# Performance work log

Measured on AMD Instinct MI355X. Metric: run time of the kernel, lower is better.

The kernel has to match this reference:

```python
import jax, jax.numpy as jnp
import numpy as np

K_NEIGHBOURS = 16
ITERATIONS = 3
NUM_CLASSES = 20
N_POINTS = 20000


def setup_inputs() -> dict:
    key = jax.random.key(0)
    k1, k2 = jax.random.split(key)
    logits = jax.random.normal(k1, (N_POINTS, NUM_CLASSES), dtype=jnp.float32)
    coords = jax.random.uniform(k2, (N_POINTS, 3), dtype=jnp.float32)
    # nn.init.eye_ then *= -0.1
    compat_w = (-0.1 * jnp.eye(NUM_CLASSES, dtype=jnp.float32))
    return {"logits": logits, "coords": coords, "compat_w": compat_w}


def _knn_graph(coords, k):
    # torch.cdist (p=2): euclidean distances, (N, N)
    sq = jnp.sum(coords * coords, axis=-1)
    d2 = sq[:, None] + sq[None, :] - 2.0 * (coords @ coords.T)
    dists = jnp.sqrt(jnp.clip(d2, 0.0))
    # smallest-k -> top_k of negated distances
    _, idx = jax.lax.top_k(-dists, k)  # (N, k)
    return idx


def reference(logits, coords, compat_w):
    knn_idx = _knn_graph(coords, K_NEIGHBOURS)
    q = jax.nn.softmax(logits, axis=-1)
    for _ in range(ITERATIONS):
        neighbour_q = q[knn_idx]            # (N, k, K) gather
        msg = jnp.mean(neighbour_q, axis=1)  # (N, K)
        refined = logits + msg @ compat_w.T  # nn.Linear: x @ W^T
        q = jax.nn.softmax(refined, axis=-1)
    return (refined, q)
```

## Files before the change

kernel.cpp:

```cpp
#include <hip/hip_runtime.h>

#define N_PTS 20000
#define NCLS 20
#define KNN 16
#define GRID 12
#define NCELLS (GRID * GRID * GRID)
#define HCELL (1.0f / (float)GRID)
#define CAND_CAP 512
#define KEY_CAP 128
#define R_TARGET 0.0680f

__device__ __forceinline__ int cell1d(float v) {
    int c = (int)(v * (float)GRID);
    return min(max(c, 0), GRID - 1);
}

__global__ __launch_bounds__(256) void count_scan_kernel(const float* __restrict__ coords,
                                                         int* __restrict__ cellCount,
                                                         int* __restrict__ doneCtr,
                                                         int* __restrict__ cellStart,
                                                         int* __restrict__ cellCursor) {
    const int p = blockIdx.x * blockDim.x + threadIdx.x;
    if (p < N_PTS) {
        const int cx = cell1d(coords[3 * p + 0]);
        const int cy = cell1d(coords[3 * p + 1]);
        const int cz = cell1d(coords[3 * p + 2]);
        atomicAdd(&cellCount[(cz * GRID + cy) * GRID + cx], 1);
    }
    __threadfence();
    __syncthreads();
    __shared__ bool isLast;
    if (threadIdx.x == 0)
        isLast = (atomicAdd(doneCtr, 1) == (int)gridDim.x - 1);
    __syncthreads();
    if (!isLast) return;

    __shared__ int part[256];
    const int t = threadIdx.x;
    const int base = t * 7;
    int local[7];
    int s = 0;
#pragma unroll
    for (int i = 0; i < 7; ++i) {
        const int c = base + i;
        const int v = (c < NCELLS)
            ? __hip_atomic_load(&cellCount[c], __ATOMIC_RELAXED, __HIP_MEMORY_SCOPE_AGENT)
            : 0;
        local[i] = s;
        s += v;
    }
    part[t] = s;
    __syncthreads();
    for (int off = 1; off < 256; off <<= 1) {
        const int v = part[t] + ((t >= off) ? part[t - off] : 0);
        __syncthreads();
        part[t] = v;
        __syncthreads();
    }
    const int excl = (t > 0) ? part[t - 1] : 0;
#pragma unroll
    for (int i = 0; i < 7; ++i) {
        const int c = base + i;
        if (c < NCELLS) {
            cellStart[c] = excl + local[i];
            cellCursor[c] = excl + local[i];
        }
    }
    if (t == 255) cellStart[NCELLS] = part[255];
}

__global__ __launch_bounds__(256) void scatter_kernel(const float* __restrict__ coords,
                                                      const float* __restrict__ logits,
                                                      int* __restrict__ cellCursor,
                                                      float4* __restrict__ sortedPts,
                                                      int* __restrict__ orig,
                                                      float* __restrict__ ls,
                                                      float* __restrict__ q0s) {
    const int p = blockIdx.x * blockDim.x + threadIdx.x;
    if (p >= N_PTS) return;
    const float x = coords[3 * p + 0];
    const float y = coords[3 * p + 1];
    const float z = coords[3 * p + 2];
    const int c = (cell1d(z) * GRID + cell1d(y)) * GRID + cell1d(x);
    const int pos = atomicAdd(&cellCursor[c], 1);
    sortedPts[pos] = make_float4(x, y, z, __uint_as_float((unsigned)p));
    orig[pos] = p;
    const float4* l4 = (const float4*)(logits + p * NCLS);
    float v[NCLS];
#pragma unroll
    for (int u = 0; u < 5; ++u) {
        const float4 a = l4[u];
        v[4 * u + 0] = a.x; v[4 * u + 1] = a.y;
        v[4 * u + 2] = a.z; v[4 * u + 3] = a.w;
    }
    float4* d4 = (float4*)(ls + pos * NCLS);
#pragma unroll
    for (int u = 0; u < 5; ++u)
        d4[u] = make_float4(v[4 * u], v[4 * u + 1], v[4 * u + 2], v[4 * u + 3]);
    float mx = v[0];
#pragma unroll
    for (int cc = 1; cc < NCLS; ++cc) mx = fmaxf(mx, v[cc]);
    float sum = 0.f;
#pragma unroll
    for (int cc = 0; cc < NCLS; ++cc) { v[cc] = __expf(v[cc] - mx); sum += v[cc]; }
    const float inv = 1.f / sum;
    float4* q4 = (float4*)(q0s + pos * NCLS);
#pragma unroll
    for (int u = 0; u < 5; ++u)
        q4[u] = make_float4(v[4 * u] * inv, v[4 * u + 1] * inv,
                            v[4 * u + 2] * inv, v[4 * u + 3] * inv);
}

__device__ void knn_ladder(const float4* __restrict__ sortedPts,
                           const int* __restrict__ cellStart,
                           const float4 qp, const int s, int hw,
                           unsigned long long* keys, const int lane,
                           int* __restrict__ knn_out) {
    const unsigned long long laneLt = (1ull << lane) - 1ull;
    const int cx = cell1d(qp.x), cy = cell1d(qp.y), cz = cell1d(qp.z);
    float g = 0.9995f * (float)hw * HCELL;
    float tau = g * g;
    int cnt = 0;
    for (int att = 0; att < 16; ++att) {
        cnt = 0;
        const int xlo = max(cx - hw, 0), xhi = min(cx + hw, GRID - 1);
        const int ylo = max(cy - hw, 0), yhi = min(cy + hw, GRID - 1);
        const int zlo = max(cz - hw, 0), zhi = min(cz + hw, GRID - 1);
        for (int zz = zlo; zz <= zhi; ++zz) {
            for (int yy = ylo; yy <= yhi; ++yy) {
                const int rowc = (zz * GRID + yy) * GRID;
                const int beg = cellStart[rowc + xlo];
                const int end = cellStart[rowc + xhi + 1];
                for (int j0 = beg; j0 < end; j0 += 64) {
                    const int j = j0 + lane;
                    const bool jv = j < end;
                    const float4 pt = sortedPts[jv ? j : beg];
                    const float dx = pt.x - qp.x, dy = pt.y - qp.y, dz = pt.z - qp.z;
                    const float d2 = dx * dx + dy * dy + dz * dz;
                    const bool take = jv && (d2 < tau);
                    const unsigned long long mm = __ballot(take);
                    if (take) {
                        const int pos = cnt + (int)__popcll(mm & laneLt);
                        if (pos < KEY_CAP)
                            keys[pos] = (((unsigned long long)__float_as_uint(d2)) << 32) |
                                        (unsigned long long)(unsigned)j;
                    }
                    cnt += (int)__popcll(mm);
                }
            }
        }
        if (cnt >= KNN && cnt <= KEY_CAP) break;
        if (cnt < KNN) {
            if (hw < GRID - 1) { ++hw; g = 0.9995f * (float)hw * HCELL; tau = g * g; }
            else tau *= 2.5f;
        } else {
            tau *= 0.6f;
        }
    }
    const int m = min(cnt, KEY_CAP);
    const unsigned long long k0 = (lane < m) ? keys[lane] : ~0ull;
    const unsigned long long k1 = (lane + 64 < m) ? keys[lane + 64] : ~0ull;
    int r0 = 0, r1 = 0;
    for (int j = 0; j < m; ++j) {
        const unsigned long long kj = keys[j];
        r0 += (kj < k0); r1 += (kj < k1);
    }
    if (lane < m && r0 < KNN)      knn_out[s * KNN + r0] = (int)(unsigned)(k0 & 0xffffffffull);
    if (lane + 64 < m && r1 < KNN) knn_out[s * KNN + r1] = (int)(unsigned)(k1 & 0xffffffffull);
}

__global__ __launch_bounds__(256) void knn_kernel(const float4* __restrict__ sortedPts,
                                                  const int* __restrict__ cellStart,
                                                  int* __restrict__ knn_out) {
    __shared__ float4 cand[CAND_CAP];
    __shared__ unsigned long long keys[4][KEY_CAP];
    const int lane = threadIdx.x & 63;
    const int wave = threadIdx.x >> 6;
    const int c = blockIdx.x >> 1;
    const int half = blockIdx.x & 1;
    const int cz = c / (GRID * GRID);
    const int cy = (c / GRID) % GRID;
    const int cx = c % GRID;
    const int pbeg = cellStart[c];
    const int pend = cellStart[c + 1];
    const int npts = pend - pbeg;
    if (npts <= 0) return;
    const unsigned long long laneLt = (1ull << lane) - 1ull;

    const int xlo = max(cx - 1, 0), xhi = min(cx + 1, GRID - 1);
    const int ylo = max(cy - 1, 0), yhi = min(cy + 1, GRID - 1);
    const int zlo = max(cz - 1, 0), zhi = min(cz + 1, GRID - 1);
    const int ny = yhi - ylo + 1;
    const int nruns = (zhi - zlo + 1) * ny;

    int beg = 0, len = 0;
    if (lane < nruns) {
        const int zz = zlo + lane / ny;
        const int yy = ylo + lane % ny;
        const int rowc = (zz * GRID + yy) * GRID;
        beg = cellStart[rowc + xlo];
        len = cellStart[rowc + xhi + 1] - beg;
    }
    int off = len;
#pragma unroll
    for (int sh = 1; sh < 16; sh <<= 1) {
        const int o = __shfl_up(off, sh, 64);
        if (lane >= sh) off += o;
    }
    const int nc = __shfl(off, nruns - 1);
    off -= len;
    const int ownRun = (cz - zlo) * ny + (cy - ylo);
    const int ownOff = __shfl(off, ownRun) + (pbeg - __shfl(beg, ownRun));

    if (nc <= CAND_CAP) {
        for (int r = wave; r < nruns; r += 4) {
            const int rb = __shfl(beg, r);
            const int rl = __shfl(len, r);
            const int ro = __shfl(off, r);
            for (int i = lane; i < rl; i += 64) {
                float4 pt = sortedPts[rb + i];
                pt.w = __uint_as_float((unsigned)(rb + i));
                cand[ro + i] = pt;
            }
        }
    }
    __syncthreads();

    if (nc > CAND_CAP) {
        for (int idx = 2 * wave + half; idx < npts; idx += 8)
            knn_ladder(sortedPts, cellStart, sortedPts[pbeg + idx], pbeg + idx,
                       2, keys[wave], lane, knn_out);
        return;
    }

    const float taumaxr = 0.9995f * HCELL;
    const float taumax = taumaxr * taumaxr;

    for (int idx = 2 * wave + half; idx < npts; idx += 8) {
        const int s = pbeg + idx;
        const float4 qp = cand[ownOff + idx];
        float r = R_TARGET;
        const float inv2r = 0.5f / r;
        const float fx = (fminf(qp.x + r, 1.f) - fmaxf(qp.x - r, 0.f)) * inv2r;
        const float fy = (fminf(qp.y + r, 1.f) - fmaxf(qp.y - r, 0.f)) * inv2r;
        const float fz = (fminf(qp.z + r, 1.f) - fmaxf(qp.z - r, 0.f)) * inv2r;
        const float f = fmaxf(fx * fy * fz, 0.05f);
        r = R_TARGET * __powf(f, -0.33333334f);
        float tau = fminf(r * r, taumax);
        bool triedMax = (tau >= taumax * 0.999f);

        int cnt = 0;
        bool ok = false;
        for (int att = 0; att < 5 && !ok; ++att) {
            cnt = 0;
            for (int j0 = 0; j0 < nc; j0 += 64) {
                const int j = j0 + lane;
                float d2 = 1e30f;
                unsigned pw = 0;
                if (j < nc) {
                    const float4 pt = cand[j];
                    const float dx = pt.x - qp.x, dy = pt.y - qp.y, dz = pt.z - qp.z;
                    d2 = dx * dx + dy * dy + dz * dz;
                    pw = __float_as_uint(pt.w);
                }
                const bool take = d2 < tau;
                const unsigned long long mm = __ballot(take);
                if (take) {
                    const int pos = cnt + (int)__popcll(mm & laneLt);
                    if (pos < KEY_CAP)
                        keys[wave][pos] =
                            (((unsigned long long)__float_as_uint(d2)) << 32) |
                            (unsigned long long)pw;
                }
                cnt += (int)__popcll(mm);
            }
            if (cnt >= KNN && cnt <= KEY_CAP) ok = true;
            else if (cnt < KNN) {
                if (triedMax) break;
                tau = taumax; triedMax = true;
            } else tau *= 0.6f;
        }
        if (!ok) {
            knn_ladder(sortedPts, cellStart, qp, s, 2, keys[wave], lane, knn_out);
            continue;
        }
        const int m = cnt;
        const unsigned long long k0 = (lane < m) ? keys[wave][lane] : ~0ull;
        const unsigned long long k1 = (lane + 64 < m) ? keys[wave][lane + 64] : ~0ull;
        int r0 = 0, r1 = 0;
        for (int j = 0; j < m; ++j) {
            const unsigned long long kj = keys[wave][j];
            r0 += (kj < k0); r1 += (kj < k1);
        }
        if (lane < m && r0 < KNN)      knn_out[s * KNN + r0] = (int)(unsigned)(k0 & 0xffffffffull);
        if (lane + 64 < m && r1 < KNN) knn_out[s * KNN + r1] = (int)(unsigned)(k1 & 0xffffffffull);
    }
}

__global__ __launch_bounds__(256) void crf_iter_kernel(const float* __restrict__ ls,
                                                       const float* __restrict__ W,
                                                       const int* __restrict__ knn,
                                                       const float* __restrict__ qin,
                                                       float* __restrict__ qout,
                                                       const int* __restrict__ orig,
                                                       float* __restrict__ outRef,
                                                       float* __restrict__ outQ) {
    __shared__ float Ws[NCLS * NCLS];
    for (int i = threadIdx.x; i < NCLS * NCLS; i += blockDim.x) Ws[i] = W[i];
    __syncthreads();
    const int t = blockIdx.x * blockDim.x + threadIdx.x;
    const int p = t >> 2;
    const int qtr = t & 3;
    if (p >= N_PTS) return;

    float acc[NCLS];
#pragma unroll
    for (int c = 0; c < NCLS; ++c) acc[c] = 0.f;

    const int4 k4 = ((const int4*)(knn + p * KNN))[qtr];
    const int ids[4] = {k4.x, k4.y, k4.z, k4.w};
#pragma unroll
    for (int u = 0; u < 4; ++u) {
        unsigned id = (unsigned)ids[u];
        if (id >= N_PTS) id = 0;
        const float4* r4 = (const float4*)(qin + id * NCLS);
#pragma unroll
        for (int v = 0; v < 5; ++v) {
            const float4 a = r4[v];
            acc[4 * v + 0] += a.x; acc[4 * v + 1] += a.y;
            acc[4 * v + 2] += a.z; acc[4 * v + 3] += a.w;
        }
    }
#pragma unroll
    for (int c = 0; c < NCLS; ++c) {
        acc[c] += __shfl_xor(acc[c], 1, 64);
        acc[c] += __shfl_xor(acc[c], 2, 64);
        acc[c] *= (1.f / 16.f);
    }

    const int c0 = qtr * 5;
    float ref[5];
#pragma unroll
    for (int i = 0; i < 5; ++i) {
        float s = ls[p * NCLS + c0 + i];
#pragma unroll
        for (int k = 0; k < NCLS; ++k) s += acc[k] * Ws[(c0 + i) * NCLS + k];
        ref[i] = s;
    }

    float mx = ref[0];
#pragma unroll
    for (int i = 1; i < 5; ++i) mx = fmaxf(mx, ref[i]);
    mx = fmaxf(mx, __shfl_xor(mx, 1, 64));
    mx = fmaxf(mx, __shfl_xor(mx, 2, 64));
    float ex[5];
    float ps = 0.f;
#pragma unroll
    for (int i = 0; i < 5; ++i) { ex[i] = __expf(ref[i] - mx); ps += ex[i]; }
    ps += __shfl_xor(ps, 1, 64);
    ps += __shfl_xor(ps, 2, 64);
    const float inv = 1.f / ps;

    if (outRef != nullptr) {
        const int o = orig[p];
#pragma unroll
        for (int i = 0; i < 5; ++i) {
            outRef[o * NCLS + c0 + i] = ref[i];
            outQ[o * NCLS + c0 + i] = ex[i] * inv;
        }
    } else {
#pragma unroll
        for (int i = 0; i < 5; ++i) qout[p * NCLS + c0 + i] = ex[i] * inv;
    }
}

extern "C" void kernel_launch(void* const* d_in, const int* in_sizes, int n_in,
                              void* d_out, int out_size, void* d_ws, size_t ws_size,
                              hipStream_t stream) {
    const float* logits = (const float*)d_in[0];
    const float* coords = (const float*)d_in[1];
    const float* W      = (const float*)d_in[2];
    float* out = (float*)d_out;

    char* ws = (char*)d_ws;
    size_t off = 0;
    int* knn = (int*)(ws + off);              off += (size_t)N_PTS * KNN * 4;
    off = (off + 255) & ~(size_t)255;
    float* ls = (float*)(ws + off);           off += (size_t)N_PTS * NCLS * 4;
    off = (off + 255) & ~(size_t)255;
    float* q0s = (float*)(ws + off);          off += (size_t)N_PTS * NCLS * 4;
    off = (off + 255) & ~(size_t)255;
    float4* sortedPts = (float4*)(ws + off);  off += (size_t)N_PTS * 16;
    off = (off + 255) & ~(size_t)255;
    int* orig = (int*)(ws + off);             off += (size_t)N_PTS * 4;
    off = (off + 255) & ~(size_t)255;
    int* cellCount = (int*)(ws + off);        off += (size_t)(NCELLS + 1) * 4;
    int* doneCtr = cellCount + NCELLS;
    off = (off + 255) & ~(size_t)255;
    int* cellStart = (int*)(ws + off);        off += (size_t)(NCELLS + 1) * 4;
    off = (off + 255) & ~(size_t)255;
    int* cellCursor = (int*)(ws + off);
    float* q1s = out + N_PTS * NCLS;

    const int threads = 256;
    const int pblocks = (N_PTS + threads - 1) / threads;
    const int cblocks = (4 * N_PTS + threads - 1) / threads;

    hipMemsetAsync(cellCount, 0, (NCELLS + 1) * sizeof(int), stream);
    count_scan_kernel<<<pblocks, threads, 0, stream>>>(coords, cellCount, doneCtr,
                                                       cellStart, cellCursor);
    scatter_kernel<<<pblocks, threads, 0, stream>>>(coords, logits, cellCursor,
                                                    sortedPts, orig, ls, q0s);
    knn_kernel<<<NCELLS * 2, threads, 0, stream>>>(sortedPts, cellStart, knn);
    crf_iter_kernel<<<cblocks, threads, 0, stream>>>(ls, W, knn, q0s, q1s, orig,
                                                     nullptr, nullptr);
    crf_iter_kernel<<<cblocks, threads, 0, stream>>>(ls, W, knn, q1s, q0s, orig,
                                                     nullptr, nullptr);
    crf_iter_kernel<<<cblocks, threads, 0, stream>>>(ls, W, knn, q0s, nullptr, orig,
                                                     out, out + N_PTS * NCLS);
}
```

Baseline: 129.7 us.

## Defer KNN fallback queries to a separate load-balanced slow kernel

Queries that fail the fast shared-memory candidate search, or sit in cells whose neighbourhood overflows the candidate cache, are appended to a global fail list through atomics instead of being handled inline with the ladder search. A new kernel then processes that list with one wave per query across 512 blocks. The aim is to remove tail imbalance, where a few blocks stall on expensive ladder searches, and to lighten register pressure in the fast kernel. The cost is an extra launch, atomics, and a fail-list buffer in the workspace.

```diff
diff --git a/kernel.cpp b/kernel.cpp
--- a/kernel.cpp
+++ b/kernel.cpp
@@ -111,67 +111,11 @@
                             v[4 * u + 2] * inv, v[4 * u + 3] * inv);
 }
 
-__device__ void knn_ladder(const float4* __restrict__ sortedPts,
-                           const int* __restrict__ cellStart,
-                           const float4 qp, const int s, int hw,
-                           unsigned long long* keys, const int lane,
-                           int* __restrict__ knn_out) {
-    const unsigned long long laneLt = (1ull << lane) - 1ull;
-    const int cx = cell1d(qp.x), cy = cell1d(qp.y), cz = cell1d(qp.z);
-    float g = 0.9995f * (float)hw * HCELL;
-    float tau = g * g;
-    int cnt = 0;
-    for (int att = 0; att < 16; ++att) {
-        cnt = 0;
-        const int xlo = max(cx - hw, 0), xhi = min(cx + hw, GRID - 1);
-        const int ylo = max(cy - hw, 0), yhi = min(cy + hw, GRID - 1);
-        const int zlo = max(cz - hw, 0), zhi = min(cz + hw, GRID - 1);
-        for (int zz = zlo; zz <= zhi; ++zz) {
-            for (int yy = ylo; yy <= yhi; ++yy) {
-                const int rowc = (zz * GRID + yy) * GRID;
-                const int beg = cellStart[rowc + xlo];
-                const int end = cellStart[rowc + xhi + 1];
-                for (int j0 = beg; j0 < end; j0 += 64) {
-                    const int j = j0 + lane;
-                    const bool jv = j < end;
-                    const float4 pt = sortedPts[jv ? j : beg];
-                    const float dx = pt.x - qp.x, dy = pt.y - qp.y, dz = pt.z - qp.z;
-                    const float d2 = dx * dx + dy * dy + dz * dz;
-                    const bool take = jv && (d2 < tau);
-                    const unsigned long long mm = __ballot(take);
-                    if (take) {
-                        const int pos = cnt + (int)__popcll(mm & laneLt);
-                        if (pos < KEY_CAP)
-                            keys[pos] = (((unsigned long long)__float_as_uint(d2)) << 32) |
-                                        (unsigned long long)(unsigned)j;
-                    }
-                    cnt += (int)__popcll(mm);
-                }
-            }
-        }
-        if (cnt >= KNN && cnt <= KEY_CAP) break;
-        if (cnt < KNN) {
-            if (hw < GRID - 1) { ++hw; g = 0.9995f * (float)hw * HCELL; tau = g * g; }
-            else tau *= 2.5f;
-        } else {
-            tau *= 0.6f;
-        }
-    }
-    const int m = min(cnt, KEY_CAP);
-    const unsigned long long k0 = (lane < m) ? keys[lane] : ~0ull;
-    const unsigned long long k1 = (lane + 64 < m) ? keys[lane + 64] : ~0ull;
-    int r0 = 0, r1 = 0;
-    for (int j = 0; j < m; ++j) {
-        const unsigned long long kj = keys[j];
-        r0 += (kj < k0); r1 += (kj < k1);
-    }
-    if (lane < m && r0 < KNN)      knn_out[s * KNN + r0] = (int)(unsigned)(k0 & 0xffffffffull);
-    if (lane + 64 < m && r1 < KNN) knn_out[s * KNN + r1] = (int)(unsigned)(k1 & 0xffffffffull);
-}
-
 __global__ __launch_bounds__(256) void knn_kernel(const float4* __restrict__ sortedPts,
                                                   const int* __restrict__ cellStart,
-                                                  int* __restrict__ knn_out) {
+                                                  int* __restrict__ knn_out,
+                                                  int* __restrict__ failList,
+                                                  int* __restrict__ failCount) {
     __shared__ float4 cand[CAND_CAP];
     __shared__ unsigned long long keys[4][KEY_CAP];
     const int lane = threadIdx.x & 63;
@@ -212,26 +156,26 @@
     const int ownRun = (cz - zlo) * ny + (cy - ylo);
     const int ownOff = __shfl(off, ownRun) + (pbeg - __shfl(beg, ownRun));
 
-    if (nc <= CAND_CAP) {
-        for (int r = wave; r < nruns; r += 4) {
-            const int rb = __shfl(beg, r);
-            const int rl = __shfl(len, r);
-            const int ro = __shfl(off, r);
-            for (int i = lane; i < rl; i += 64) {
-                float4 pt = sortedPts[rb + i];
-                pt.w = __uint_as_float((unsigned)(rb + i));
-                cand[ro + i] = pt;
-            }
+    if (nc > CAND_CAP) {
+        if (threadIdx.x == 0) {
+            const int nmine = (npts - half + 1) / 2;
+            int b = atomicAdd(failCount, nmine);
+            for (int idx = half; idx < npts; idx += 2) failList[b++] = pbeg + idx;
+        }
+        return;
+    }
+
+    for (int r = wave; r < nruns; r += 4) {
+        const int rb = __shfl(beg, r);
+        const int rl = __shfl(len, r);
+        const int ro = __shfl(off, r);
+        for (int i = lane; i < rl; i += 64) {
+            float4 pt = sortedPts[rb + i];
+            pt.w = __uint_as_float((unsigned)(rb + i));
+            cand[ro + i] = pt;
         }
     }
     __syncthreads();
-
-    if (nc > CAND_CAP) {
-        for (int idx = 2 * wave + half; idx < npts; idx += 8)
-            knn_ladder(sortedPts, cellStart, sortedPts[pbeg + idx], pbeg + idx,
-                       2, keys[wave], lane, knn_out);
-        return;
-    }
 
     const float taumaxr = 0.9995f * HCELL;
     const float taumax = taumaxr * taumaxr;
@@ -281,10 +225,81 @@
             } else tau *= 0.6f;
         }
         if (!ok) {
-            knn_ladder(sortedPts, cellStart, qp, s, 2, keys[wave], lane, knn_out);
+            if (lane == 0) { const int b = atomicAdd(failCount, 1); failList[b] = s; }
             continue;
         }
         const int m = cnt;
+        const unsigned long long k0 = (lane < m) ? keys[wave][lane] : ~0ull;
+        const unsigned long long k1 = (lane + 64 < m) ? keys[wave][lane + 64] : ~0ull;
+        int r0 = 0, r1 = 0;
+        for (int j = 0; j < m; ++j) {
+            const unsigned long long kj = keys[wave][j];
+            r0 += (kj < k0); r1 += (kj < k1);
+        }
+        if (lane < m && r0 < KNN)      knn_out[s * KNN + r0] = (int)(unsigned)(k0 & 0xffffffffull);
+        if (lane + 64 < m && r1 < KNN) knn_out[s * KNN + r1] = (int)(unsigned)(k1 & 0xffffffffull);
+    }
+}
+
+__global__ __launch_bounds__(256) void knn_slow_kernel(const float4* __restrict__ sortedPts,
+                                                       const int* __restrict__ cellStart,
+                                                       const int* __restrict__ failList,
+                                                       const int* __restrict__ failCount,
+                                                       int* __restrict__ knn_out) {
+    __shared__ unsigned long long keys[4][KEY_CAP];
+    const int lane = threadIdx.x & 63;
+    const int wave = threadIdx.x >> 6;
+    const int wid = blockIdx.x * 4 + wave;
+    const int nw = gridDim.x * 4;
+    const int nf = failCount[0];
+    const unsigned long long laneLt = (1ull << lane) - 1ull;
+
+    for (int fi = wid; fi < nf; fi += nw) {
+        const int s = failList[fi];
+        const float4 qp = sortedPts[s];
+        const int cx = cell1d(qp.x), cy = cell1d(qp.y), cz = cell1d(qp.z);
+        int hw = 2;
+        float g = 0.9995f * 2.f * HCELL;
+        float tau = g * g;
+        int cnt = 0;
+        for (int att = 0; att < 16; ++att) {
+            cnt = 0;
+            const int xlo = max(cx - hw, 0), xhi = min(cx + hw, GRID - 1);
+            const int ylo = max(cy - hw, 0), yhi = min(cy + hw, GRID - 1);
+            const int zlo = max(cz - hw, 0), zhi = min(cz + hw, GRID - 1);
+            for (int zz = zlo; zz <= zhi; ++zz) {
+                for (int yy = ylo; yy <= yhi; ++yy) {
+                    const int rowc = (zz * GRID + yy) * GRID;
+                    const int beg = cellStart[rowc + xlo];
+                    const int end = cellStart[rowc + xhi + 1];
+                    for (int j0 = beg; j0 < end; j0 += 64) {
+                        const int j = j0 + lane;
+                        const bool jv = j < end;
+                        const float4 pt = sortedPts[jv ? j : beg];
+                        const float dx = pt.x - qp.x, dy = pt.y - qp.y, dz = pt.z - qp.z;
+                        const float d2 = dx * dx + dy * dy + dz * dz;
+                        const bool take = jv && (d2 < tau);
+                        const unsigned long long mm = __ballot(take);
+                        if (take) {
+                            const int pos = cnt + (int)__popcll(mm & laneLt);
+                            if (pos < KEY_CAP)
+                                keys[wave][pos] =
+                                    (((unsigned long long)__float_as_uint(d2)) << 32) |
+                                    (unsigned long long)(unsigned)j;
+                        }
+                        cnt += (int)__popcll(mm);
+                    }
+                }
+            }
+            if (cnt >= KNN && cnt <= KEY_CAP) break;
+            if (cnt < KNN) {
+                if (hw < GRID - 1) { ++hw; g = 0.9995f * (float)hw * HCELL; tau = g * g; }
+                else tau *= 2.5f;
+            } else {
+                tau *= 0.6f;
+            }
+        }
+        const int m = min(cnt, KEY_CAP);
         const unsigned long long k0 = (lane < m) ? keys[wave][lane] : ~0ull;
         const unsigned long long k1 = (lane + 64 < m) ? keys[wave][lane + 64] : ~0ull;
         int r0 = 0, r1 = 0;
@@ -394,8 +409,11 @@
     off = (off + 255) & ~(size_t)255;
     int* orig = (int*)(ws + off);             off += (size_t)N_PTS * 4;
     off = (off + 255) & ~(size_t)255;
-    int* cellCount = (int*)(ws + off);        off += (size_t)(NCELLS + 1) * 4;
+    int* failList = (int*)(ws + off);         off += (size_t)N_PTS * 4;
+    off = (off + 255) & ~(size_t)255;
+    int* cellCount = (int*)(ws + off);        off += (size_t)(NCELLS + 2) * 4;
     int* doneCtr = cellCount + NCELLS;
+    int* failCount = cellCount + NCELLS + 1;
     off = (off + 255) & ~(size_t)255;
     int* cellStart = (int*)(ws + off);        off += (size_t)(NCELLS + 1) * 4;
     off = (off + 255) & ~(size_t)255;
@@ -406,12 +424,15 @@
     const int pblocks = (N_PTS + threads - 1) / threads;
     const int cblocks = (4 * N_PTS + threads - 1) / threads;
 
-    hipMemsetAsync(cellCount, 0, (NCELLS + 1) * sizeof(int), stream);
+    hipMemsetAsync(cellCount, 0, (NCELLS + 2) * sizeof(int), stream);
     count_scan_kernel<<<pblocks, threads, 0, stream>>>(coords, cellCount, doneCtr,
                                                        cellStart, cellCursor);
     scatter_kernel<<<pblocks, threads, 0, stream>>>(coords, logits, cellCursor,
                                                     sortedPts, orig, ls, q0s);
-    knn_kernel<<<NCELLS * 2, threads, 0, stream>>>(sortedPts, cellStart, knn);
+    knn_kernel<<<NCELLS * 2, threads, 0, stream>>>(sortedPts, cellStart, knn,
+                                                   failList, failCount);
+    knn_slow_kernel<<<512, threads, 0, stream>>>(sortedPts, cellStart, failList,
+                                                 failCount, knn);
     crf_iter_kernel<<<cblocks, threads, 0, stream>>>(ls, W, knn, q0s, q1s, orig,
                                                      nullptr, nullptr);
     crf_iter_kernel<<<cblocks, threads, 0, stream>>>(ls, W, knn, q1s, q0s, orig,
```

Result: slower. 147.7 us (+13.9%).
